# Kernel optimization log

Measured on AMD Instinct MI355X. Metric: run time of the kernel, lower is better.

Reference implementation:

```python
import jax, jax.numpy as jnp
import numpy as np

HEADS = 8
NEG_SLOPE = 0.2  # PyG GATConv default negative_slope


def segment_softmax(logits, seg, num_segments):
    # logits: [E, H], seg: [E] destination ids
    m = jax.ops.segment_max(logits, seg, num_segments=num_segments)
    m = jnp.where(jnp.isfinite(m), m, 0.0)
    e = jnp.exp(logits - jax.lax.stop_gradient(m)[seg])
    s = jax.ops.segment_sum(e, seg, num_segments=num_segments)
    return e / (s[seg] + 1e-16)


def setup_inputs() -> dict:
    key = jax.random.key(0)
    k1, k2, k3, k4, k5, k6 = jax.random.split(key, 6)
    N, F_IN, H, C, E = 50000, 116, HEADS, 32, 800000
    x = jax.random.normal(k1, (N, F_IN), dtype=jnp.float32)
    edge_index = jax.random.randint(k2, (2, E), 0, N, dtype=jnp.int64)
    # Params (glorot-ish scale)
    W = jax.random.normal(k3, (F_IN, H * C), dtype=jnp.float32) * (1.0 / np.sqrt(F_IN))
    att_src = jax.random.normal(k4, (1, H, C), dtype=jnp.float32) * (1.0 / np.sqrt(C))
    att_dst = jax.random.normal(k5, (1, H, C), dtype=jnp.float32) * (1.0 / np.sqrt(C))
    bias = jnp.zeros((C,), dtype=jnp.float32)
    return {"x": x, "edge_index": edge_index, "W": W, "att_src": att_src, "att_dst": att_dst, "bias": bias}


def reference(x, edge_index, W, att_src, att_dst, bias):
    N = x.shape[0]
    H = HEADS
    C = W.shape[1] // H
    # Shared linear transform: [N, H, C]
    xt = (x @ W).reshape(N, H, C)
    alpha_src = jnp.sum(xt * att_src, axis=-1)  # [N, H]
    alpha_dst = jnp.sum(xt * att_dst, axis=-1)  # [N, H]
    # add_self_loops=True (PyG GATConv default)
    loops = jnp.arange(N, dtype=edge_index.dtype)
    src = jnp.concatenate([edge_index[0], loops])
    dst = jnp.concatenate([edge_index[1], loops])
    # Edge-wise attention logits + segment softmax over destination
    alpha = jax.nn.leaky_relu(alpha_src[src] + alpha_dst[dst], negative_slope=NEG_SLOPE)  # [E', H]
    alpha = segment_softmax(alpha, dst, N)
    # Weighted message aggregation
    msg = xt[src] * alpha[:, :, None]  # [E', H, C]
    out = jax.ops.segment_sum(msg, dst, num_segments=N)  # [N, H, C]
    # concat=False -> mean over heads, then bias
    out = out.mean(axis=1) + bias  # [N, C]
    return jax.nn.relu(out)
```

## Files before the change

kernel.cpp:

```cpp
#include <hip/hip_runtime.h>
#include <hip/hip_bf16.h>


#define F_IN 116
#define HC 256
#define NHEAD 8
#define CDIM 32
#define KP 128
#define ROWS_PB 48
#define DSLOT 64
#define ECHUNK 4096

typedef unsigned int uint32;
typedef short short8 __attribute__((ext_vector_type(8)));
typedef float f32x4 __attribute__((ext_vector_type(4)));

__device__ __forceinline__ unsigned short f2bf(float f) {
    uint32 u = __float_as_uint(f);
    u = (u + 0x7FFF + ((u >> 16) & 1)) >> 16;
    return (unsigned short)u;
}

__global__ void init_k(const float* __restrict__ W,
                       const float* __restrict__ att_s,
                       const float* __restrict__ att_d,
                       unsigned short* __restrict__ WbT,
                       unsigned short* __restrict__ WaT,
                       int* __restrict__ cnt, int N) {
    int idx = blockIdx.x * 256 + threadIdx.x;
    for (int i = idx; i < N; i += 144 * 256) cnt[i] = 0;
    if (idx < 32768) {
        int n = idx >> 7, k = idx & 127;
        WbT[idx] = (k < F_IN) ? f2bf(W[k * HC + n]) : (unsigned short)0;
    } else {
        int aid = idx - 32768;
        int col = aid >> 7, k = aid & 127;
        int tile = col >> 4;
        int cc = col & 15;
        int h = cc & 7, part = cc >> 3;
        const float* att = tile ? att_d : att_s;
        float s = 0.f;
        if (k < F_IN) {
            for (int c = 0; c < CDIM; ++c)
                s = fmaf(W[k * HC + h * CDIM + c], att[h * CDIM + c], s);
        }
        unsigned short hi = f2bf(s);
        unsigned short v = hi;
        if (part) {
            float rem = s - __uint_as_float((uint32)hi << 16);
            v = f2bf(rem);
        }
        WaT[col * KP + k] = v;
    }
}

__global__ __launch_bounds__(256) void fuse_k(const float* __restrict__ x,
                                              const unsigned short* __restrict__ WbT,
                                              const unsigned short* __restrict__ WaT,
                                              unsigned short* __restrict__ xth,
                                              float* __restrict__ asrc,
                                              float* __restrict__ adst,
                                              int N, int nScatGrp, int Ggemm,
                                              const int* __restrict__ src,
                                              const int* __restrict__ dst,
                                              int* __restrict__ cnt,
                                              unsigned short* __restrict__ csr, int E) {
    const int t = threadIdx.x;
    const int g = blockIdx.x >> 3, r = blockIdx.x & 7;
    const int c = g / 5, p = g - c * 5;

    if (p < 3) {
        const int sg = c * 3 + p;
        if (sg >= nScatGrp) return;
        const int sbid = sg * 8 + r;
        const int slice = sbid & 7;
        const int chunk = sbid >> 3;
        const int SLICE = (N + 7) >> 3;
        const int lo = slice * SLICE;
        const int hi = (lo + SLICE < N) ? lo + SLICE : N;
        const int ebase = chunk * ECHUNK + t * 4;
#pragma unroll
        for (int it = 0; it < ECHUNK / 1024; ++it) {
            int e = ebase + it * 1024;
            if (e < E) {
                int4 d4 = *(const int4*)&dst[e];
                int4 s4 = *(const int4*)&src[e];
                if (d4.x >= lo && d4.x < hi) {
                    int rr = atomicAdd(&cnt[d4.x], 1);
                    if (rr < DSLOT) csr[(d4.x << 6) + rr] = (unsigned short)s4.x;
                }
                if (d4.y >= lo && d4.y < hi) {
                    int rr = atomicAdd(&cnt[d4.y], 1);
                    if (rr < DSLOT) csr[(d4.y << 6) + rr] = (unsigned short)s4.y;
                }
                if (d4.z >= lo && d4.z < hi) {
                    int rr = atomicAdd(&cnt[d4.z], 1);
                    if (rr < DSLOT) csr[(d4.z << 6) + rr] = (unsigned short)s4.z;
                }
                if (d4.w >= lo && d4.w < hi) {
                    int rr = atomicAdd(&cnt[d4.w], 1);
                    if (rr < DSLOT) csr[(d4.w << 6) + rr] = (unsigned short)s4.w;
                }
            }
        }
        return;
    }

    const int gbid = (c * 2 + (p - 3)) * 8 + r;
    if (gbid >= Ggemm) return;

    __shared__ unsigned short xbs[16 * ROWS_PB * 8];
    const int row0 = gbid * ROWS_PB;
    for (int u = t; u < 16 * ROWS_PB; u += 256) {
        const int gg = u / ROWS_PB, rr = u - gg * ROWS_PB;
        const int gr = row0 + rr;
        f32x4 v0 = {0.f, 0.f, 0.f, 0.f}, v1 = {0.f, 0.f, 0.f, 0.f};
        if (gr < N) {
            const f32x4* xp = (const f32x4*)(x + (size_t)gr * F_IN + gg * 8);
            if (gg < 14) { v0 = xp[0]; v1 = xp[1]; }
            else if (gg == 14) { v0 = xp[0]; }
        }
        short8 pk;
        pk[0] = (short)f2bf(v0.x); pk[1] = (short)f2bf(v0.y);
        pk[2] = (short)f2bf(v0.z); pk[3] = (short)f2bf(v0.w);
        pk[4] = (short)f2bf(v1.x); pk[5] = (short)f2bf(v1.y);
        pk[6] = (short)f2bf(v1.z); pk[7] = (short)f2bf(v1.w);
        *(short8*)&xbs[u * 8] = pk;
    }
    __syncthreads();

    const int w = t >> 6, l = t & 63;
    const int q = l >> 4, m = l & 15;
    const int ncol0 = w * 64;

    short8 bfr[4][4];
#pragma unroll
    for (int nt = 0; nt < 4; ++nt)
#pragma unroll
        for (int ks = 0; ks < 4; ++ks)
            bfr[nt][ks] = *(const short8*)&WbT[(size_t)(ncol0 + nt * 16 + m) * KP + ks * 32 + q * 8];

    short8 wa[4];
    if (w < 2) {
#pragma unroll
        for (int ks = 0; ks < 4; ++ks)
            wa[ks] = *(const short8*)&WaT[(size_t)(w * 16 + m) * KP + ks * 32 + q * 8];
    }

    f32x4 acc[3][4];
#pragma unroll
    for (int rt = 0; rt < 3; ++rt)
#pragma unroll
        for (int nt = 0; nt < 4; ++nt) acc[rt][nt] = f32x4{0.f, 0.f, 0.f, 0.f};
    f32x4 acc_a[3];
#pragma unroll
    for (int rt = 0; rt < 3; ++rt) acc_a[rt] = f32x4{0.f, 0.f, 0.f, 0.f};

#pragma unroll
    for (int ks = 0; ks < 4; ++ks) {
        short8 a[3];
#pragma unroll
        for (int rt = 0; rt < 3; ++rt)
            a[rt] = *(const short8*)&xbs[((ks * 4 + q) * ROWS_PB + rt * 16 + m) * 8];
#pragma unroll
        for (int nt = 0; nt < 4; ++nt)
#pragma unroll
            for (int rt = 0; rt < 3; ++rt)
                acc[rt][nt] = __builtin_amdgcn_mfma_f32_16x16x32_bf16(bfr[nt][ks], a[rt], acc[rt][nt], 0, 0, 0);
        if (w < 2) {
#pragma unroll
            for (int rt = 0; rt < 3; ++rt)
                acc_a[rt] = __builtin_amdgcn_mfma_f32_16x16x32_bf16(wa[ks], a[rt], acc_a[rt], 0, 0, 0);
        }
    }

#pragma unroll
    for (int rt = 0; rt < 3; ++rt) {
        const int row = row0 + rt * 16 + m;
        if (row < N) {
#pragma unroll
            for (int nt = 0; nt < 4; ++nt) {
                uint2 pk;
                pk.x = (uint32)f2bf(acc[rt][nt][0]) | ((uint32)f2bf(acc[rt][nt][1]) << 16);
                pk.y = (uint32)f2bf(acc[rt][nt][2]) | ((uint32)f2bf(acc[rt][nt][3]) << 16);
                *(uint2*)&xth[(size_t)row * HC + ncol0 + nt * 16 + q * 4] = pk;
            }
        }
    }

    if (w < 2) {
        float* ap = (w == 0) ? asrc : adst;
#pragma unroll
        for (int rt = 0; rt < 3; ++rt) {
            f32x4 s;
#pragma unroll
            for (int rr = 0; rr < 4; ++rr) {
                float v = acc_a[rt][rr];
                s[rr] = v + __shfl_xor(v, 32, 64);
            }
            const int row = row0 + rt * 16 + m;
            if (q < 2 && row < N)
                *(f32x4*)&ap[row * NHEAD + q * 4] = s;
        }
    }
}

__global__ __launch_bounds__(256) void aggregate_k(const unsigned short* __restrict__ xth,
                                                   const float* __restrict__ asrc,
                                                   const float* __restrict__ adst,
                                                   const int* __restrict__ cnt,
                                                   const unsigned short* __restrict__ csr,
                                                   const float* __restrict__ bias,
                                                   float* __restrict__ out, int N) {
    const int t = threadIdx.x;
    const int lg = t & 31;
    const int base = t & 32;
    const int n = blockIdx.x * 8 + (t >> 5);
    if (n >= N) return;

    const int h_f = lg >> 2;
    const int h_w = lg & 7;
    const int e_w = lg >> 3;

    const int beg = n << 6;
    int d = cnt[n];
    if (d > DSLOT) d = DSLOT;

    const float adst_hw = adst[n * NHEAD + h_w];

    float zs = asrc[n * NHEAD + h_f] + adst[n * NHEAD + h_f];
    zs = (zs > 0.f) ? zs : 0.2f * zs;
    const float wself = __expf(zs);

    uint4 sv = ((const uint4*)(xth + (size_t)n * HC))[lg];
    float a0 = wself * __uint_as_float(sv.x << 16);
    float a1 = wself * __uint_as_float(sv.x & 0xFFFF0000u);
    float a2 = wself * __uint_as_float(sv.y << 16);
    float a3 = wself * __uint_as_float(sv.y & 0xFFFF0000u);
    float a4 = wself * __uint_as_float(sv.z << 16);
    float a5 = wself * __uint_as_float(sv.z & 0xFFFF0000u);
    float a6 = wself * __uint_as_float(sv.w << 16);
    float a7 = wself * __uint_as_float(sv.w & 0xFFFF0000u);
    float wsum = wself;

    const int nfull = d >> 2;
    const int rem = d & 3;
    int pos = beg;
    for (int cch = 0; cch < nfull; ++cch, pos += 4) {
        int s_w = (int)csr[pos + e_w];
        float z = asrc[s_w * NHEAD + h_w] + adst_hw;
        z = (z > 0.f) ? z : 0.2f * z;
        float w_reg = __expf(z);
#pragma unroll
        for (int e = 0; e < 4; ++e) {
            int s = __shfl(s_w, base + (e << 3), 64);
            float w = __shfl(w_reg, base + (e << 3) + h_f, 64);
            uint4 v = ((const uint4*)(xth + (size_t)s * HC))[lg];
            a0 = fmaf(w, __uint_as_float(v.x << 16), a0);
            a1 = fmaf(w, __uint_as_float(v.x & 0xFFFF0000u), a1);
            a2 = fmaf(w, __uint_as_float(v.y << 16), a2);
            a3 = fmaf(w, __uint_as_float(v.y & 0xFFFF0000u), a3);
            a4 = fmaf(w, __uint_as_float(v.z << 16), a4);
            a5 = fmaf(w, __uint_as_float(v.z & 0xFFFF0000u), a5);
            a6 = fmaf(w, __uint_as_float(v.w << 16), a6);
            a7 = fmaf(w, __uint_as_float(v.w & 0xFFFF0000u), a7);
            wsum += w;
        }
    }
    if (rem) {
        int s_w = (e_w < rem) ? (int)csr[pos + e_w] : n;
        float z = asrc[s_w * NHEAD + h_w] + adst_hw;
        z = (z > 0.f) ? z : 0.2f * z;
        float w_reg = __expf(z);
        for (int e = 0; e < rem; ++e) {
            int s = __shfl(s_w, base + (e << 3), 64);
            float w = __shfl(w_reg, base + (e << 3) + h_f, 64);
            uint4 v = ((const uint4*)(xth + (size_t)s * HC))[lg];
            a0 = fmaf(w, __uint_as_float(v.x << 16), a0);
            a1 = fmaf(w, __uint_as_float(v.x & 0xFFFF0000u), a1);
            a2 = fmaf(w, __uint_as_float(v.y << 16), a2);
            a3 = fmaf(w, __uint_as_float(v.y & 0xFFFF0000u), a3);
            a4 = fmaf(w, __uint_as_float(v.z << 16), a4);
            a5 = fmaf(w, __uint_as_float(v.z & 0xFFFF0000u), a5);
            a6 = fmaf(w, __uint_as_float(v.w << 16), a6);
            a7 = fmaf(w, __uint_as_float(v.w & 0xFFFF0000u), a7);
            wsum += w;
        }
    }

    const float inv = 1.f / (wsum + 1e-16f);
    a0 *= inv; a1 *= inv; a2 *= inv; a3 *= inv;
    a4 *= inv; a5 *= inv; a6 *= inv; a7 *= inv;

#pragma unroll
    for (int o = 4; o <= 16; o <<= 1) {
        a0 += __shfl_xor(a0, o, 64);
        a1 += __shfl_xor(a1, o, 64);
        a2 += __shfl_xor(a2, o, 64);
        a3 += __shfl_xor(a3, o, 64);
        a4 += __shfl_xor(a4, o, 64);
        a5 += __shfl_xor(a5, o, 64);
        a6 += __shfl_xor(a6, o, 64);
        a7 += __shfl_xor(a7, o, 64);
    }

    if (lg < 4) {
        const float* bp = bias + 8 * lg;
        float4 r0, r1;
        r0.x = fmaxf(a0 * 0.125f + bp[0], 0.f);
        r0.y = fmaxf(a1 * 0.125f + bp[1], 0.f);
        r0.z = fmaxf(a2 * 0.125f + bp[2], 0.f);
        r0.w = fmaxf(a3 * 0.125f + bp[3], 0.f);
        r1.x = fmaxf(a4 * 0.125f + bp[4], 0.f);
        r1.y = fmaxf(a5 * 0.125f + bp[5], 0.f);
        r1.z = fmaxf(a6 * 0.125f + bp[6], 0.f);
        r1.w = fmaxf(a7 * 0.125f + bp[7], 0.f);
        *(float4*)&out[(size_t)n * CDIM + 8 * lg] = r0;
        *(float4*)&out[(size_t)n * CDIM + 8 * lg + 4] = r1;
    }
}

extern "C" void kernel_launch(void* const* d_in, const int* in_sizes, int n_in,
                              void* d_out, int out_size, void* d_ws, size_t ws_size,
                              hipStream_t stream) {
    const float* x     = (const float*)d_in[0];
    const int*   ei    = (const int*)d_in[1];
    const float* W     = (const float*)d_in[2];
    const float* att_s = (const float*)d_in[3];
    const float* att_d = (const float*)d_in[4];
    const float* bias  = (const float*)d_in[5];
    float* out = (float*)d_out;

    const int N = in_sizes[0] / F_IN;
    const int E = in_sizes[1] / 2;

    unsigned short* xth = (unsigned short*)d_ws;
    unsigned short* WbT = xth + (size_t)N * HC;
    float* asrc = (float*)(WbT + 256 * KP);
    float* adst = asrc + (size_t)N * NHEAD;
    int*   cnt  = (int*)(adst + (size_t)N * NHEAD);
    unsigned short* csr = (unsigned short*)(cnt + N);
    unsigned short* WaT = csr + (size_t)N * DSLOT;

    const int Ggemm = (N + ROWS_PB - 1) / ROWS_PB;
    const int nchunk = (E + ECHUNK - 1) / ECHUNK;
    const int Gscat = nchunk * 8;
    const int nScatGrp = (Gscat + 7) / 8;
    const int nGemmGrp = (Ggemm + 7) / 8;
    const int cS = (nScatGrp + 2) / 3;
    const int cG = (nGemmGrp + 1) / 2;
    const int ncyc = (cS > cG) ? cS : cG;
    const int Gfuse = ncyc * 5 * 8;

    init_k<<<144, 256, 0, stream>>>(W, att_s, att_d, WbT, WaT, cnt, N);
    fuse_k<<<Gfuse, 256, 0, stream>>>(x, WbT, WaT, xth, asrc, adst,
                                      N, nScatGrp, Ggemm,
                                      ei, ei + E, cnt, csr, E);
    aggregate_k<<<(N + 7) / 8, 256, 0, stream>>>(xth, asrc, adst, cnt, csr, bias, out, N);
}
```

Baseline: 201.3 us.

## Merge init, GEMM/scatter and aggregation into one cooperative persistent kernel

Replaces the three kernel launches with a single cooperative kernel that runs the init, the interleaved GEMM and CSR scatter, and the aggregation as phases separated by grid-wide syncs. Blocks loop persistently over work items, and odd and even blocks swap the order of GEMM and scatter so the two overlap. The aim is to remove launch gaps and per-kernel tail effects. In exchange it adds grid-sync overhead, caps the grid at 1024 blocks of limited occupancy, and calls the occupancy and device-property queries on the host at every launch.

```diff
diff --git a/kernel.cpp b/kernel.cpp
--- a/kernel.cpp
+++ b/kernel.cpp
@@ -1,5 +1,6 @@
 #include <hip/hip_runtime.h>
 #include <hip/hip_bf16.h>
+#include <hip/hip_cooperative_groups.h>
 
 
 #define F_IN 116
@@ -15,308 +16,311 @@
 typedef short short8 __attribute__((ext_vector_type(8)));
 typedef float f32x4 __attribute__((ext_vector_type(4)));
 
+namespace cg = cooperative_groups;
+
 __device__ __forceinline__ unsigned short f2bf(float f) {
     uint32 u = __float_as_uint(f);
     u = (u + 0x7FFF + ((u >> 16) & 1)) >> 16;
     return (unsigned short)u;
 }
 
-__global__ void init_k(const float* __restrict__ W,
-                       const float* __restrict__ att_s,
-                       const float* __restrict__ att_d,
-                       unsigned short* __restrict__ WbT,
-                       unsigned short* __restrict__ WaT,
-                       int* __restrict__ cnt, int N) {
-    int idx = blockIdx.x * 256 + threadIdx.x;
-    for (int i = idx; i < N; i += 144 * 256) cnt[i] = 0;
-    if (idx < 32768) {
-        int n = idx >> 7, k = idx & 127;
-        WbT[idx] = (k < F_IN) ? f2bf(W[k * HC + n]) : (unsigned short)0;
-    } else {
-        int aid = idx - 32768;
-        int col = aid >> 7, k = aid & 127;
-        int tile = col >> 4;
-        int cc = col & 15;
-        int h = cc & 7, part = cc >> 3;
-        const float* att = tile ? att_d : att_s;
-        float s = 0.f;
-        if (k < F_IN) {
-            for (int c = 0; c < CDIM; ++c)
-                s = fmaf(W[k * HC + h * CDIM + c], att[h * CDIM + c], s);
-        }
-        unsigned short hi = f2bf(s);
-        unsigned short v = hi;
-        if (part) {
-            float rem = s - __uint_as_float((uint32)hi << 16);
-            v = f2bf(rem);
-        }
-        WaT[col * KP + k] = v;
+__global__ __launch_bounds__(256, 4) void gat_k(
+        const float* __restrict__ x,
+        const int* __restrict__ src,
+        const int* __restrict__ dst,
+        const float* __restrict__ W,
+        const float* __restrict__ att_s,
+        const float* __restrict__ att_d,
+        const float* __restrict__ bias,
+        unsigned short* __restrict__ WbT,
+        unsigned short* __restrict__ WaT,
+        unsigned short* __restrict__ xth,
+        float* __restrict__ asrc,
+        float* __restrict__ adst,
+        int* __restrict__ cnt,
+        unsigned short* __restrict__ csr,
+        float* __restrict__ out,
+        int N, int E, int nchunk, int Ggemm, int NG) {
+    const int t = threadIdx.x;
+    const int b = blockIdx.x;
+    const int G = gridDim.x;
+    __shared__ unsigned short xbs[16 * ROWS_PB * 8];
+
+    for (int i = b * 256 + t; i < N; i += G * 256) cnt[i] = 0;
+    for (int idx = b * 256 + t; idx < 36864; idx += G * 256) {
+        if (idx < 32768) {
+            int n = idx >> 7, k = idx & 127;
+            WbT[idx] = (k < F_IN) ? f2bf(W[k * HC + n]) : (unsigned short)0;
+        } else {
+            int aid = idx - 32768;
+            int col = aid >> 7, k = aid & 127;
+            int tile = col >> 4;
+            int cc = col & 15;
+            int h = cc & 7, part = cc >> 3;
+            const float* att = tile ? att_d : att_s;
+            float s = 0.f;
+            if (k < F_IN) {
+                for (int c = 0; c < CDIM; ++c)
+                    s = fmaf(W[k * HC + h * CDIM + c], att[h * CDIM + c], s);
+            }
+            unsigned short hi = f2bf(s);
+            unsigned short v = hi;
+            if (part) {
+                float rem = s - __uint_as_float((uint32)hi << 16);
+                v = f2bf(rem);
+            }
+            WaT[col * KP + k] = v;
+        }
     }
-}
-
-__global__ __launch_bounds__(256) void fuse_k(const float* __restrict__ x,
-                                              const unsigned short* __restrict__ WbT,
-                                              const unsigned short* __restrict__ WaT,
-                                              unsigned short* __restrict__ xth,
-                                              float* __restrict__ asrc,
-                                              float* __restrict__ adst,
-                                              int N, int nScatGrp, int Ggemm,
-                                              const int* __restrict__ src,
-                                              const int* __restrict__ dst,
-                                              int* __restrict__ cnt,
-                                              unsigned short* __restrict__ csr, int E) {
-    const int t = threadIdx.x;
-    const int g = blockIdx.x >> 3, r = blockIdx.x & 7;
-    const int c = g / 5, p = g - c * 5;
-
-    if (p < 3) {
-        const int sg = c * 3 + p;
-        if (sg >= nScatGrp) return;
-        const int sbid = sg * 8 + r;
-        const int slice = sbid & 7;
-        const int chunk = sbid >> 3;
+    cg::this_grid().sync();
+
+    auto do_scatter = [&]() {
+        const int slice = b & 7;
         const int SLICE = (N + 7) >> 3;
         const int lo = slice * SLICE;
         const int hi = (lo + SLICE < N) ? lo + SLICE : N;
-        const int ebase = chunk * ECHUNK + t * 4;
-#pragma unroll
-        for (int it = 0; it < ECHUNK / 1024; ++it) {
-            int e = ebase + it * 1024;
-            if (e < E) {
-                int4 d4 = *(const int4*)&dst[e];
-                int4 s4 = *(const int4*)&src[e];
-                if (d4.x >= lo && d4.x < hi) {
-                    int rr = atomicAdd(&cnt[d4.x], 1);
-                    if (rr < DSLOT) csr[(d4.x << 6) + rr] = (unsigned short)s4.x;
-                }
-                if (d4.y >= lo && d4.y < hi) {
-                    int rr = atomicAdd(&cnt[d4.y], 1);
-                    if (rr < DSLOT) csr[(d4.y << 6) + rr] = (unsigned short)s4.y;
-                }
-                if (d4.z >= lo && d4.z < hi) {
-                    int rr = atomicAdd(&cnt[d4.z], 1);
-                    if (rr < DSLOT) csr[(d4.z << 6) + rr] = (unsigned short)s4.z;
-                }
-                if (d4.w >= lo && d4.w < hi) {
-                    int rr = atomicAdd(&cnt[d4.w], 1);
-                    if (rr < DSLOT) csr[(d4.w << 6) + rr] = (unsigned short)s4.w;
-                }
-            }
-        }
-        return;
-    }
-
-    const int gbid = (c * 2 + (p - 3)) * 8 + r;
-    if (gbid >= Ggemm) return;
-
-    __shared__ unsigned short xbs[16 * ROWS_PB * 8];
-    const int row0 = gbid * ROWS_PB;
-    for (int u = t; u < 16 * ROWS_PB; u += 256) {
-        const int gg = u / ROWS_PB, rr = u - gg * ROWS_PB;
-        const int gr = row0 + rr;
-        f32x4 v0 = {0.f, 0.f, 0.f, 0.f}, v1 = {0.f, 0.f, 0.f, 0.f};
-        if (gr < N) {
-            const f32x4* xp = (const f32x4*)(x + (size_t)gr * F_IN + gg * 8);
-            if (gg < 14) { v0 = xp[0]; v1 = xp[1]; }
-            else if (gg == 14) { v0 = xp[0]; }
-        }
-        short8 pk;
-        pk[0] = (short)f2bf(v0.x); pk[1] = (short)f2bf(v0.y);
-        pk[2] = (short)f2bf(v0.z); pk[3] = (short)f2bf(v0.w);
-        pk[4] = (short)f2bf(v1.x); pk[5] = (short)f2bf(v1.y);
-        pk[6] = (short)f2bf(v1.z); pk[7] = (short)f2bf(v1.w);
-        *(short8*)&xbs[u * 8] = pk;
-    }
-    __syncthreads();
-
-    const int w = t >> 6, l = t & 63;
-    const int q = l >> 4, m = l & 15;
-    const int ncol0 = w * 64;
-
-    short8 bfr[4][4];
-#pragma unroll
-    for (int nt = 0; nt < 4; ++nt)
-#pragma unroll
-        for (int ks = 0; ks < 4; ++ks)
-            bfr[nt][ks] = *(const short8*)&WbT[(size_t)(ncol0 + nt * 16 + m) * KP + ks * 32 + q * 8];
-
-    short8 wa[4];
-    if (w < 2) {
-#pragma unroll
-        for (int ks = 0; ks < 4; ++ks)
-            wa[ks] = *(const short8*)&WaT[(size_t)(w * 16 + m) * KP + ks * 32 + q * 8];
-    }
-
-    f32x4 acc[3][4];
-#pragma unroll
-    for (int rt = 0; rt < 3; ++rt)
-#pragma unroll
-        for (int nt = 0; nt < 4; ++nt) acc[rt][nt] = f32x4{0.f, 0.f, 0.f, 0.f};
-    f32x4 acc_a[3];
-#pragma unroll
-    for (int rt = 0; rt < 3; ++rt) acc_a[rt] = f32x4{0.f, 0.f, 0.f, 0.f};
-
-#pragma unroll
-    for (int ks = 0; ks < 4; ++ks) {
-        short8 a[3];
-#pragma unroll
-        for (int rt = 0; rt < 3; ++rt)
-            a[rt] = *(const short8*)&xbs[((ks * 4 + q) * ROWS_PB + rt * 16 + m) * 8];
-#pragma unroll
-        for (int nt = 0; nt < 4; ++nt)
+        const int Gs = G >> 3;
+        for (int c = b >> 3; c < nchunk; c += Gs) {
+            const int ebase = c * ECHUNK + t * 4;
+#pragma unroll
+            for (int it = 0; it < ECHUNK / 1024; ++it) {
+                int e = ebase + it * 1024;
+                if (e < E) {
+                    int4 d4 = *(const int4*)&dst[e];
+                    int4 s4 = *(const int4*)&src[e];
+                    if (d4.x >= lo && d4.x < hi) {
+                        int rr = atomicAdd(&cnt[d4.x], 1);
+                        if (rr < DSLOT) csr[(d4.x << 6) + rr] = (unsigned short)s4.x;
+                    }
+                    if (d4.y >= lo && d4.y < hi) {
+                        int rr = atomicAdd(&cnt[d4.y], 1);
+                        if (rr < DSLOT) csr[(d4.y << 6) + rr] = (unsigned short)s4.y;
+                    }
+                    if (d4.z >= lo && d4.z < hi) {
+                        int rr = atomicAdd(&cnt[d4.z], 1);
+                        if (rr < DSLOT) csr[(d4.z << 6) + rr] = (unsigned short)s4.z;
+                    }
+                    if (d4.w >= lo && d4.w < hi) {
+                        int rr = atomicAdd(&cnt[d4.w], 1);
+                        if (rr < DSLOT) csr[(d4.w << 6) + rr] = (unsigned short)s4.w;
+                    }
+                }
+            }
+        }
+    };
+
+    auto do_gemm = [&]() {
+        for (int g = b; g < Ggemm; g += G) {
+            __syncthreads();
+            const int row0 = g * ROWS_PB;
+            for (int u = t; u < 16 * ROWS_PB; u += 256) {
+                const int gg = u / ROWS_PB, rr = u - gg * ROWS_PB;
+                const int gr = row0 + rr;
+                f32x4 v0 = {0.f, 0.f, 0.f, 0.f}, v1 = {0.f, 0.f, 0.f, 0.f};
+                if (gr < N) {
+                    const f32x4* xp = (const f32x4*)(x + (size_t)gr * F_IN + gg * 8);
+                    if (gg < 14) { v0 = xp[0]; v1 = xp[1]; }
+                    else if (gg == 14) { v0 = xp[0]; }
+                }
+                short8 pk;
+                pk[0] = (short)f2bf(v0.x); pk[1] = (short)f2bf(v0.y);
+                pk[2] = (short)f2bf(v0.z); pk[3] = (short)f2bf(v0.w);
+                pk[4] = (short)f2bf(v1.x); pk[5] = (short)f2bf(v1.y);
+                pk[6] = (short)f2bf(v1.z); pk[7] = (short)f2bf(v1.w);
+                *(short8*)&xbs[u * 8] = pk;
+            }
+            __syncthreads();
+
+            const int w = t >> 6, l = t & 63;
+            const int q = l >> 4, m = l & 15;
+            const int ncol0 = w * 64;
+
+            short8 bfr[4][4];
+#pragma unroll
+            for (int nt = 0; nt < 4; ++nt)
+#pragma unroll
+                for (int ks = 0; ks < 4; ++ks)
+                    bfr[nt][ks] = *(const short8*)&WbT[(size_t)(ncol0 + nt * 16 + m) * KP + ks * 32 + q * 8];
+
+            short8 wa[4];
+            if (w < 2) {
+#pragma unroll
+                for (int ks = 0; ks < 4; ++ks)
+                    wa[ks] = *(const short8*)&WaT[(size_t)(w * 16 + m) * KP + ks * 32 + q * 8];
+            }
+
+            f32x4 acc[3][4];
 #pragma unroll
             for (int rt = 0; rt < 3; ++rt)
-                acc[rt][nt] = __builtin_amdgcn_mfma_f32_16x16x32_bf16(bfr[nt][ks], a[rt], acc[rt][nt], 0, 0, 0);
-        if (w < 2) {
-#pragma unroll
-            for (int rt = 0; rt < 3; ++rt)
-                acc_a[rt] = __builtin_amdgcn_mfma_f32_16x16x32_bf16(wa[ks], a[rt], acc_a[rt], 0, 0, 0);
-        }
-    }
-
-#pragma unroll
-    for (int rt = 0; rt < 3; ++rt) {
-        const int row = row0 + rt * 16 + m;
-        if (row < N) {
-#pragma unroll
-            for (int nt = 0; nt < 4; ++nt) {
-                uint2 pk;
-                pk.x = (uint32)f2bf(acc[rt][nt][0]) | ((uint32)f2bf(acc[rt][nt][1]) << 16);
-                pk.y = (uint32)f2bf(acc[rt][nt][2]) | ((uint32)f2bf(acc[rt][nt][3]) << 16);
-                *(uint2*)&xth[(size_t)row * HC + ncol0 + nt * 16 + q * 4] = pk;
-            }
-        }
-    }
-
-    if (w < 2) {
-        float* ap = (w == 0) ? asrc : adst;
-#pragma unroll
-        for (int rt = 0; rt < 3; ++rt) {
-            f32x4 s;
-#pragma unroll
-            for (int rr = 0; rr < 4; ++rr) {
-                float v = acc_a[rt][rr];
-                s[rr] = v + __shfl_xor(v, 32, 64);
-            }
-            const int row = row0 + rt * 16 + m;
-            if (q < 2 && row < N)
-                *(f32x4*)&ap[row * NHEAD + q * 4] = s;
-        }
-    }
-}
-
-__global__ __launch_bounds__(256) void aggregate_k(const unsigned short* __restrict__ xth,
-                                                   const float* __restrict__ asrc,
-                                                   const float* __restrict__ adst,
-                                                   const int* __restrict__ cnt,
-                                                   const unsigned short* __restrict__ csr,
-                                                   const float* __restrict__ bias,
-                                                   float* __restrict__ out, int N) {
-    const int t = threadIdx.x;
-    const int lg = t & 31;
-    const int base = t & 32;
-    const int n = blockIdx.x * 8 + (t >> 5);
-    if (n >= N) return;
-
-    const int h_f = lg >> 2;
-    const int h_w = lg & 7;
-    const int e_w = lg >> 3;
-
-    const int beg = n << 6;
-    int d = cnt[n];
-    if (d > DSLOT) d = DSLOT;
-
-    const float adst_hw = adst[n * NHEAD + h_w];
-
-    float zs = asrc[n * NHEAD + h_f] + adst[n * NHEAD + h_f];
-    zs = (zs > 0.f) ? zs : 0.2f * zs;
-    const float wself = __expf(zs);
-
-    uint4 sv = ((const uint4*)(xth + (size_t)n * HC))[lg];
-    float a0 = wself * __uint_as_float(sv.x << 16);
-    float a1 = wself * __uint_as_float(sv.x & 0xFFFF0000u);
-    float a2 = wself * __uint_as_float(sv.y << 16);
-    float a3 = wself * __uint_as_float(sv.y & 0xFFFF0000u);
-    float a4 = wself * __uint_as_float(sv.z << 16);
-    float a5 = wself * __uint_as_float(sv.z & 0xFFFF0000u);
-    float a6 = wself * __uint_as_float(sv.w << 16);
-    float a7 = wself * __uint_as_float(sv.w & 0xFFFF0000u);
-    float wsum = wself;
-
-    const int nfull = d >> 2;
-    const int rem = d & 3;
-    int pos = beg;
-    for (int cch = 0; cch < nfull; ++cch, pos += 4) {
-        int s_w = (int)csr[pos + e_w];
-        float z = asrc[s_w * NHEAD + h_w] + adst_hw;
-        z = (z > 0.f) ? z : 0.2f * z;
-        float w_reg = __expf(z);
-#pragma unroll
-        for (int e = 0; e < 4; ++e) {
-            int s = __shfl(s_w, base + (e << 3), 64);
-            float w = __shfl(w_reg, base + (e << 3) + h_f, 64);
-            uint4 v = ((const uint4*)(xth + (size_t)s * HC))[lg];
-            a0 = fmaf(w, __uint_as_float(v.x << 16), a0);
-            a1 = fmaf(w, __uint_as_float(v.x & 0xFFFF0000u), a1);
-            a2 = fmaf(w, __uint_as_float(v.y << 16), a2);
-            a3 = fmaf(w, __uint_as_float(v.y & 0xFFFF0000u), a3);
-            a4 = fmaf(w, __uint_as_float(v.z << 16), a4);
-            a5 = fmaf(w, __uint_as_float(v.z & 0xFFFF0000u), a5);
-            a6 = fmaf(w, __uint_as_float(v.w << 16), a6);
-            a7 = fmaf(w, __uint_as_float(v.w & 0xFFFF0000u), a7);
-            wsum += w;
-        }
-    }
-    if (rem) {
-        int s_w = (e_w < rem) ? (int)csr[pos + e_w] : n;
-        float z = asrc[s_w * NHEAD + h_w] + adst_hw;
-        z = (z > 0.f) ? z : 0.2f * z;
-        float w_reg = __expf(z);
-        for (int e = 0; e < rem; ++e) {
-            int s = __shfl(s_w, base + (e << 3), 64);
-            float w = __shfl(w_reg, base + (e << 3) + h_f, 64);
-            uint4 v = ((const uint4*)(xth + (size_t)s * HC))[lg];
-            a0 = fmaf(w, __uint_as_float(v.x << 16), a0);
-            a1 = fmaf(w, __uint_as_float(v.x & 0xFFFF0000u), a1);
-            a2 = fmaf(w, __uint_as_float(v.y << 16), a2);
-            a3 = fmaf(w, __uint_as_float(v.y & 0xFFFF0000u), a3);
-            a4 = fmaf(w, __uint_as_float(v.z << 16), a4);
-            a5 = fmaf(w, __uint_as_float(v.z & 0xFFFF0000u), a5);
-            a6 = fmaf(w, __uint_as_float(v.w << 16), a6);
-            a7 = fmaf(w, __uint_as_float(v.w & 0xFFFF0000u), a7);
-            wsum += w;
-        }
-    }
-
-    const float inv = 1.f / (wsum + 1e-16f);
-    a0 *= inv; a1 *= inv; a2 *= inv; a3 *= inv;
-    a4 *= inv; a5 *= inv; a6 *= inv; a7 *= inv;
-
-#pragma unroll
-    for (int o = 4; o <= 16; o <<= 1) {
-        a0 += __shfl_xor(a0, o, 64);
-        a1 += __shfl_xor(a1, o, 64);
-        a2 += __shfl_xor(a2, o, 64);
-        a3 += __shfl_xor(a3, o, 64);
-        a4 += __shfl_xor(a4, o, 64);
-        a5 += __shfl_xor(a5, o, 64);
-        a6 += __shfl_xor(a6, o, 64);
-        a7 += __shfl_xor(a7, o, 64);
-    }
-
-    if (lg < 4) {
-        const float* bp = bias + 8 * lg;
-        float4 r0, r1;
-        r0.x = fmaxf(a0 * 0.125f + bp[0], 0.f);
-        r0.y = fmaxf(a1 * 0.125f + bp[1], 0.f);
-        r0.z = fmaxf(a2 * 0.125f + bp[2], 0.f);
-        r0.w = fmaxf(a3 * 0.125f + bp[3], 0.f);
-        r1.x = fmaxf(a4 * 0.125f + bp[4], 0.f);
-        r1.y = fmaxf(a5 * 0.125f + bp[5], 0.f);
-        r1.z = fmaxf(a6 * 0.125f + bp[6], 0.f);
-        r1.w = fmaxf(a7 * 0.125f + bp[7], 0.f);
-        *(float4*)&out[(size_t)n * CDIM + 8 * lg] = r0;
-        *(float4*)&out[(size_t)n * CDIM + 8 * lg + 4] = r1;
+#pragma unroll
+                for (int nt = 0; nt < 4; ++nt) acc[rt][nt] = f32x4{0.f, 0.f, 0.f, 0.f};
+            f32x4 acc_a[3];
+#pragma unroll
+            for (int rt = 0; rt < 3; ++rt) acc_a[rt] = f32x4{0.f, 0.f, 0.f, 0.f};
+
+#pragma unroll
+            for (int ks = 0; ks < 4; ++ks) {
+                short8 a[3];
+#pragma unroll
+                for (int rt = 0; rt < 3; ++rt)
+                    a[rt] = *(const short8*)&xbs[((ks * 4 + q) * ROWS_PB + rt * 16 + m) * 8];
+#pragma unroll
+                for (int nt = 0; nt < 4; ++nt)
+#pragma unroll
+                    for (int rt = 0; rt < 3; ++rt)
+                        acc[rt][nt] = __builtin_amdgcn_mfma_f32_16x16x32_bf16(bfr[nt][ks], a[rt], acc[rt][nt], 0, 0, 0);
+                if (w < 2) {
+#pragma unroll
+                    for (int rt = 0; rt < 3; ++rt)
+                        acc_a[rt] = __builtin_amdgcn_mfma_f32_16x16x32_bf16(wa[ks], a[rt], acc_a[rt], 0, 0, 0);
+                }
+            }
+
+#pragma unroll
+            for (int rt = 0; rt < 3; ++rt) {
+                const int row = row0 + rt * 16 + m;
+                if (row < N) {
+#pragma unroll
+                    for (int nt = 0; nt < 4; ++nt) {
+                        uint2 pk;
+                        pk.x = (uint32)f2bf(acc[rt][nt][0]) | ((uint32)f2bf(acc[rt][nt][1]) << 16);
+                        pk.y = (uint32)f2bf(acc[rt][nt][2]) | ((uint32)f2bf(acc[rt][nt][3]) << 16);
+                        *(uint2*)&xth[(size_t)row * HC + ncol0 + nt * 16 + q * 4] = pk;
+                    }
+                }
+            }
+
+            if (w < 2) {
+                float* ap = (w == 0) ? asrc : adst;
+#pragma unroll
+                for (int rt = 0; rt < 3; ++rt) {
+                    f32x4 s;
+#pragma unroll
+                    for (int rr = 0; rr < 4; ++rr) {
+                        float v = acc_a[rt][rr];
+                        s[rr] = v + __shfl_xor(v, 32, 64);
+                    }
+                    const int row = row0 + rt * 16 + m;
+                    if (q < 2 && row < N)
+                        *(f32x4*)&ap[row * NHEAD + q * 4] = s;
+                }
+            }
+        }
+    };
+
+    if (b & 1) { do_gemm(); do_scatter(); }
+    else       { do_scatter(); do_gemm(); }
+
+    cg::this_grid().sync();
+
+    for (int ng = b; ng < NG; ng += G) {
+        const int lg = t & 31;
+        const int base = t & 32;
+        const int n = ng * 8 + (t >> 5);
+        if (n >= N) continue;
+
+        const int h_f = lg >> 2;
+        const int h_w = lg & 7;
+        const int e_w = lg >> 3;
+
+        const int beg = n << 6;
+        int d;
+        if (lg == 0) d = atomicAdd(&cnt[n], 0);
+        d = __shfl(d, base, 64);
+        if (d > DSLOT) d = DSLOT;
+
+        const float adst_hw = adst[n * NHEAD + h_w];
+
+        float zs = asrc[n * NHEAD + h_f] + adst[n * NHEAD + h_f];
+        zs = (zs > 0.f) ? zs : 0.2f * zs;
+        const float wself = __expf(zs);
+
+        uint4 sv = ((const uint4*)(xth + (size_t)n * HC))[lg];
+        float a0 = wself * __uint_as_float(sv.x << 16);
+        float a1 = wself * __uint_as_float(sv.x & 0xFFFF0000u);
+        float a2 = wself * __uint_as_float(sv.y << 16);
+        float a3 = wself * __uint_as_float(sv.y & 0xFFFF0000u);
+        float a4 = wself * __uint_as_float(sv.z << 16);
+        float a5 = wself * __uint_as_float(sv.z & 0xFFFF0000u);
+        float a6 = wself * __uint_as_float(sv.w << 16);
+        float a7 = wself * __uint_as_float(sv.w & 0xFFFF0000u);
+        float wsum = wself;
+
+        const int nfull = d >> 2;
+        const int rem = d & 3;
+        int pos = beg;
+        for (int cch = 0; cch < nfull; ++cch, pos += 4) {
+            int s_w = (int)csr[pos + e_w];
+            float z = asrc[s_w * NHEAD + h_w] + adst_hw;
+            z = (z > 0.f) ? z : 0.2f * z;
+            float w_reg = __expf(z);
+#pragma unroll
+            for (int e = 0; e < 4; ++e) {
+                int s = __shfl(s_w, base + (e << 3), 64);
+                float w = __shfl(w_reg, base + (e << 3) + h_f, 64);
+                uint4 v = ((const uint4*)(xth + (size_t)s * HC))[lg];
+                a0 = fmaf(w, __uint_as_float(v.x << 16), a0);
+                a1 = fmaf(w, __uint_as_float(v.x & 0xFFFF0000u), a1);
+                a2 = fmaf(w, __uint_as_float(v.y << 16), a2);
+                a3 = fmaf(w, __uint_as_float(v.y & 0xFFFF0000u), a3);
+                a4 = fmaf(w, __uint_as_float(v.z << 16), a4);
+                a5 = fmaf(w, __uint_as_float(v.z & 0xFFFF0000u), a5);
+                a6 = fmaf(w, __uint_as_float(v.w << 16), a6);
+                a7 = fmaf(w, __uint_as_float(v.w & 0xFFFF0000u), a7);
+                wsum += w;
+            }
+        }
+        if (rem) {
+            int s_w = (e_w < rem) ? (int)csr[pos + e_w] : n;
+            float z = asrc[s_w * NHEAD + h_w] + adst_hw;
+            z = (z > 0.f) ? z : 0.2f * z;
+            float w_reg = __expf(z);
+            for (int e = 0; e < rem; ++e) {
+                int s = __shfl(s_w, base + (e << 3), 64);
+                float w = __shfl(w_reg, base + (e << 3) + h_f, 64);
+                uint4 v = ((const uint4*)(xth + (size_t)s * HC))[lg];
+                a0 = fmaf(w, __uint_as_float(v.x << 16), a0);
+                a1 = fmaf(w, __uint_as_float(v.x & 0xFFFF0000u), a1);
+                a2 = fmaf(w, __uint_as_float(v.y << 16), a2);
+                a3 = fmaf(w, __uint_as_float(v.y & 0xFFFF0000u), a3);
+                a4 = fmaf(w, __uint_as_float(v.z << 16), a4);
+                a5 = fmaf(w, __uint_as_float(v.z & 0xFFFF0000u), a5);
+                a6 = fmaf(w, __uint_as_float(v.w << 16), a6);
+                a7 = fmaf(w, __uint_as_float(v.w & 0xFFFF0000u), a7);
+                wsum += w;
+            }
+        }
+
+        const float inv = 1.f / (wsum + 1e-16f);
+        a0 *= inv; a1 *= inv; a2 *= inv; a3 *= inv;
+        a4 *= inv; a5 *= inv; a6 *= inv; a7 *= inv;
+
+#pragma unroll
+        for (int o = 4; o <= 16; o <<= 1) {
+            a0 += __shfl_xor(a0, o, 64);
+            a1 += __shfl_xor(a1, o, 64);
+            a2 += __shfl_xor(a2, o, 64);
+            a3 += __shfl_xor(a3, o, 64);
+            a4 += __shfl_xor(a4, o, 64);
+            a5 += __shfl_xor(a5, o, 64);
+            a6 += __shfl_xor(a6, o, 64);
+            a7 += __shfl_xor(a7, o, 64);
+        }
+
+        if (lg < 4) {
+            const float* bp = bias + 8 * lg;
+            float4 r0, r1;
+            r0.x = fmaxf(a0 * 0.125f + bp[0], 0.f);
+            r0.y = fmaxf(a1 * 0.125f + bp[1], 0.f);
+            r0.z = fmaxf(a2 * 0.125f + bp[2], 0.f);
+            r0.w = fmaxf(a3 * 0.125f + bp[3], 0.f);
+            r1.x = fmaxf(a4 * 0.125f + bp[4], 0.f);
+            r1.y = fmaxf(a5 * 0.125f + bp[5], 0.f);
+            r1.z = fmaxf(a6 * 0.125f + bp[6], 0.f);
+            r1.w = fmaxf(a7 * 0.125f + bp[7], 0.f);
+            *(float4*)&out[(size_t)n * CDIM + 8 * lg] = r0;
+            *(float4*)&out[(size_t)n * CDIM + 8 * lg + 4] = r1;
+        }
     }
 }
 
@@ -331,8 +335,8 @@
     const float* bias  = (const float*)d_in[5];
     float* out = (float*)d_out;
 
-    const int N = in_sizes[0] / F_IN;
-    const int E = in_sizes[1] / 2;
+    int N = in_sizes[0] / F_IN;
+    int E = in_sizes[1] / 2;
 
     unsigned short* xth = (unsigned short*)d_ws;
     unsigned short* WbT = xth + (size_t)N * HC;
@@ -342,19 +346,32 @@
     unsigned short* csr = (unsigned short*)(cnt + N);
     unsigned short* WaT = csr + (size_t)N * DSLOT;
 
-    const int Ggemm = (N + ROWS_PB - 1) / ROWS_PB;
-    const int nchunk = (E + ECHUNK - 1) / ECHUNK;
-    const int Gscat = nchunk * 8;
-    const int nScatGrp = (Gscat + 7) / 8;
-    const int nGemmGrp = (Ggemm + 7) / 8;
-    const int cS = (nScatGrp + 2) / 3;
-    const int cG = (nGemmGrp + 1) / 2;
-    const int ncyc = (cS > cG) ? cS : cG;
-    const int Gfuse = ncyc * 5 * 8;
-
-    init_k<<<144, 256, 0, stream>>>(W, att_s, att_d, WbT, WaT, cnt, N);
-    fuse_k<<<Gfuse, 256, 0, stream>>>(x, WbT, WaT, xth, asrc, adst,
-                                      N, nScatGrp, Ggemm,
-                                      ei, ei + E, cnt, csr, E);
-    aggregate_k<<<(N + 7) / 8, 256, 0, stream>>>(xth, asrc, adst, cnt, csr, bias, out, N);
+    int Ggemm  = (N + ROWS_PB - 1) / ROWS_PB;
+    int nchunk = (E + ECHUNK - 1) / ECHUNK;
+    int NG     = (N + 7) / 8;
+
+    const int* src_p = ei;
+    const int* dst_p = ei + E;
+
+    int occ = 0;
+    (void)hipOccupancyMaxActiveBlocksPerMultiprocessor(
+        &occ, reinterpret_cast<const void*>(gat_k), 256, 0);
+    if (occ < 1) occ = 1;
+    int nCU = 256;
+    hipDeviceProp_t prop;
+    if (hipGetDeviceProperties(&prop, 0) == hipSuccess && prop.multiProcessorCount > 0)
+        nCU = prop.multiProcessorCount;
+    long long Gl = (long long)occ * nCU;
+    int G = (Gl > 1024) ? 1024 : (int)Gl;
+    G &= ~7;
+    if (G < 8) G = 8;
+
+    void* args[] = {
+        (void*)&x, (void*)&src_p, (void*)&dst_p, (void*)&W, (void*)&att_s,
+        (void*)&att_d, (void*)&bias, (void*)&WbT, (void*)&WaT, (void*)&xth,
+        (void*)&asrc, (void*)&adst, (void*)&cnt, (void*)&csr, (void*)&out,
+        (void*)&N, (void*)&E, (void*)&nchunk, (void*)&Ggemm, (void*)&NG
+    };
+    (void)hipLaunchCooperativeKernel(reinterpret_cast<const void*>(gat_k),
+                                     dim3(G), dim3(256), args, 0, stream);
 }
```

Result: slower. 377.0 us (+87.3%).
